# Kernel tuning notes

Measured on AMD Instinct MI355X. Metric: run time of the kernel, lower is better.

The kernel has to match this reference:

```python
import jax, jax.numpy as jnp
import numpy as np

B, C, H, W = 4, 256, 64, 64
CQ = C // 8


def setup_inputs() -> dict:
    key = jax.random.key(0)
    ks = jax.random.split(key, 8)
    s = 0.02
    return {
        "x": jax.random.normal(ks[0], (B, C, H, W), dtype=jnp.float32),
        "Wq": jax.random.normal(ks[1], (CQ, C), dtype=jnp.float32) * s,
        "bq": jax.random.normal(ks[2], (CQ,), dtype=jnp.float32) * s,
        "Wk": jax.random.normal(ks[3], (CQ, C), dtype=jnp.float32) * s,
        "bk": jax.random.normal(ks[4], (CQ,), dtype=jnp.float32) * s,
        "Wv": jax.random.normal(ks[5], (C, C), dtype=jnp.float32) * s,
        "bv": jax.random.normal(ks[6], (C,), dtype=jnp.float32) * s,
        "gamma": jax.random.normal(ks[7], (1,), dtype=jnp.float32) * s,
    }


def reference(x, Wq, bq, Wk, bk, Wv, bv, gamma):
    b, c, h, w = x.shape
    n = h * w
    xf = x.reshape(b, c, n)  # [B,C,N]; 1x1 conv == channel matmul
    q = jnp.einsum("oc,bcn->bno", Wq, xf) + bq  # [B,N,CQ]
    k = jnp.einsum("oc,bcn->bon", Wk, xf) + bk[:, None]  # [B,CQ,N]
    v = jnp.einsum("oc,bcn->bno", Wv, xf) + bv  # [B,N,C]
    attn = jnp.einsum("bnd,bdm->bnm", q, k)  # [B,N,N], unscaled
    attn = jax.nn.softmax(attn, axis=1)  # non-standard axis (over rows)
    out = jnp.einsum("bnm,bmc->bnc", attn, v)  # [B,N,C]
    out = out.transpose(0, 2, 1).reshape(b, c, h, w)
    return gamma * out + x
```

## Files before the change

kernel.cpp:

```cpp
#include <hip/hip_runtime.h>

#define B_ 4
#define C_ 256
#define N_ 4096
#define LOG2E 1.44269504088896340736f

typedef __attribute__((ext_vector_type(8))) short bf16x8;
typedef __attribute__((ext_vector_type(4))) float f32x4;

static __device__ __forceinline__ unsigned short f2bf(float f) {
    unsigned u = __builtin_bit_cast(unsigned, f);
    u += 0x7fffu + ((u >> 16) & 1u);
    return (unsigned short)(u >> 16);
}

static __device__ __forceinline__ float fexp2(float x) {
#if __has_builtin(__builtin_amdgcn_exp2f)
    return __builtin_amdgcn_exp2f(x);
#else
    return exp2f(x);
#endif
}

#define LDS_BARRIER() asm volatile("s_waitcnt lgkmcnt(0)\n\ts_barrier" ::: "memory")

__global__ void k0_wprep(const float* __restrict__ Wq, const float* __restrict__ Wk,
                         const float* __restrict__ Wv, float* __restrict__ WqkT,
                         unsigned short* __restrict__ wvb) {
    int t = blockIdx.x * 256 + threadIdx.x;
    if (t < 256 * 64) {
        int c = t >> 6, o = t & 63;
        WqkT[t] = (o < 32) ? Wq[o * C_ + c] * LOG2E : Wk[(o - 32) * C_ + c];
    }
    int t2 = t - 256 * 64;
    if (t2 >= 0 && t2 < 256 * 256) wvb[t2] = f2bf(Wv[t2]);
}

__global__ __launch_bounds__(256) void k1_qkx(const float* __restrict__ x,
        const float* __restrict__ WqkT, const float* __restrict__ bq,
        const float* __restrict__ bk, unsigned short* __restrict__ qb,
        unsigned short* __restrict__ ktb, unsigned short* __restrict__ xb) {
    __shared__ float red[4][64][64];
    int b = blockIdx.y;
    int n0 = blockIdx.x * 64;
    int l = threadIdx.x & 63, v = threadIdx.x >> 6;
    const float* xp = x + (size_t)b * C_ * N_ + n0 + l;
    unsigned short* xbp = xb + (size_t)b * C_ * N_ + n0 + l;
    float acc[64];
#pragma unroll
    for (int o = 0; o < 64; ++o) acc[o] = 0.0f;
    for (int c = 64 * v; c < 64 * v + 64; ++c) {
        float xv = xp[(size_t)c * N_];
        xbp[(size_t)c * N_] = f2bf(xv);
        const float4* wr4 = (const float4*)(WqkT + c * 64);
#pragma unroll
        for (int o4 = 0; o4 < 16; ++o4) {
            float4 wv = wr4[o4];
            acc[4 * o4 + 0] += wv.x * xv;
            acc[4 * o4 + 1] += wv.y * xv;
            acc[4 * o4 + 2] += wv.z * xv;
            acc[4 * o4 + 3] += wv.w * xv;
        }
    }
#pragma unroll
    for (int o = 0; o < 64; ++o) red[v][l][o] = acc[o];
    __syncthreads();
    int n = threadIdx.x & 63, og = threadIdx.x >> 6;
    int o0 = og * 16;
    unsigned pk[8];
#pragma unroll
    for (int i = 0; i < 8; ++i) {
        int oa = o0 + 2 * i, ob = oa + 1;
        float va = red[0][n][oa] + red[1][n][oa] + red[2][n][oa] + red[3][n][oa];
        float vb = red[0][n][ob] + red[1][n][ob] + red[2][n][ob] + red[3][n][ob];
        if (og < 2) { va += bq[oa] * LOG2E; vb += bq[ob] * LOG2E; }
        else        { va += bk[oa - 32];    vb += bk[ob - 32]; }
        pk[i] = (unsigned)f2bf(va) | ((unsigned)f2bf(vb) << 16);
    }
    unsigned short* dst = (og < 2)
        ? qb + ((size_t)b * N_ + n0 + n) * 32 + o0
        : ktb + ((size_t)b * N_ + n0 + n) * 32 + (o0 - 32);
    ((uint4*)dst)[0] = make_uint4(pk[0], pk[1], pk[2], pk[3]);
    ((uint4*)dst)[1] = make_uint4(pk[4], pk[5], pk[6], pk[7]);
}

__global__ __launch_bounds__(512) void k2_stats(const unsigned short* __restrict__ qb,
        const unsigned short* __restrict__ ktb, float* __restrict__ Wcol) {
    __shared__ float red[64][33];
    int b = blockIdx.y;
    int m0 = blockIdx.x * 64;
    int lane = threadIdx.x & 63, w = threadIdx.x >> 6;
    int r16 = lane & 15, g = lane >> 4;
    const unsigned short* kb = ktb + ((size_t)b * N_ + m0 + r16) * 32 + 8 * g;
    bf16x8 kf0 = *(const bf16x8*)(kb);
    bf16x8 kf1 = *(const bf16x8*)(kb + 16 * 32);
    bf16x8 kf2 = *(const bf16x8*)(kb + 32 * 32);
    bf16x8 kf3 = *(const bf16x8*)(kb + 48 * 32);
    float z0 = 0, z1 = 0, z2 = 0, z3 = 0;
    const unsigned short* qbase = qb + ((size_t)b * N_ + w * 512 + r16) * 32 + 8 * g;
#pragma unroll 2
    for (int n0 = 0; n0 < 512; n0 += 16) {
        bf16x8 qf = *(const bf16x8*)(qbase + (size_t)n0 * 32);
        f32x4 d0 = __builtin_amdgcn_mfma_f32_16x16x32_bf16(qf, kf0, (f32x4){0, 0, 0, 0}, 0, 0, 0);
        f32x4 d1 = __builtin_amdgcn_mfma_f32_16x16x32_bf16(qf, kf1, (f32x4){0, 0, 0, 0}, 0, 0, 0);
        f32x4 d2 = __builtin_amdgcn_mfma_f32_16x16x32_bf16(qf, kf2, (f32x4){0, 0, 0, 0}, 0, 0, 0);
        f32x4 d3 = __builtin_amdgcn_mfma_f32_16x16x32_bf16(qf, kf3, (f32x4){0, 0, 0, 0}, 0, 0, 0);
        z0 += fexp2(d0[0]) + fexp2(d0[1]) + fexp2(d0[2]) + fexp2(d0[3]);
        z1 += fexp2(d1[0]) + fexp2(d1[1]) + fexp2(d1[2]) + fexp2(d1[3]);
        z2 += fexp2(d2[0]) + fexp2(d2[1]) + fexp2(d2[2]) + fexp2(d2[3]);
        z3 += fexp2(d3[0]) + fexp2(d3[1]) + fexp2(d3[2]) + fexp2(d3[3]);
    }
    red[r16][4 * w + g] = z0;
    red[16 + r16][4 * w + g] = z1;
    red[32 + r16][4 * w + g] = z2;
    red[48 + r16][4 * w + g] = z3;
    __syncthreads();
    if (threadIdx.x < 64) {
        float s = 0;
#pragma unroll
        for (int i = 0; i < 32; ++i) s += red[threadIdx.x][i];
        Wcol[(size_t)b * N_ + m0 + threadIdx.x] = 1.0f / s;
    }
}

__global__ __launch_bounds__(512) void k4_y(const unsigned short* __restrict__ qb,
        const unsigned short* __restrict__ ktb, const unsigned short* __restrict__ xb,
        const float* __restrict__ Wcol, unsigned short* __restrict__ Yt,
        float* __restrict__ rowP) {
    __shared__ unsigned short Pl[2][64 * 64];
    __shared__ float rpl[4][64];
    int b = blockIdx.y;
    int n0 = blockIdx.x * 64;
    int lane = threadIdx.x & 63, w = threadIdx.x >> 6;
    int ms = w >> 1, wn = w & 1;
    int r16 = lane & 15, g = lane >> 4;
    int swz = (r16 & 7) << 4;

    const unsigned short* qbp = qb + ((size_t)b * N_ + n0 + 32 * wn + r16) * 32 + 8 * g;
    bf16x8 qf0 = *(const bf16x8*)(qbp);
    bf16x8 qf1 = *(const bf16x8*)(qbp + 16 * 32);
    const unsigned short* kbp = ktb + ((size_t)b * N_ + 16 * ms + r16) * 32 + 8 * g;
    const unsigned short* xbp = xb + ((size_t)b * C_ + 32 * w + r16) * N_ + 8 * g;
    const float* izp = Wcol + (size_t)b * N_ + 16 * ms + 4 * g;

    char* pwbase = (char*)&Pl[0][0] + (32 * wn + r16) * 128 + ((32 * ms + 8 * g) ^ swz);

    f32x4 acc[4][2];
#pragma unroll
    for (int i = 0; i < 4; ++i)
#pragma unroll
        for (int j = 0; j < 2; ++j) acc[i][j] = (f32x4){0, 0, 0, 0};
    float rp0 = 0.0f, rp1 = 0.0f;

    bf16x8 ka = *(const bf16x8*)(kbp);
    bf16x8 xf[2][2], xfn[2][2];
#pragma unroll
    for (int cs = 0; cs < 2; ++cs)
#pragma unroll
        for (int ks = 0; ks < 2; ++ks)
            xf[cs][ks] = *(const bf16x8*)(xbp + (size_t)cs * 16 * N_ + 32 * ks);
    float4 iz = *(const float4*)(izp);
    {
        f32x4 s0 = __builtin_amdgcn_mfma_f32_16x16x32_bf16(ka, qf0, (f32x4){0, 0, 0, 0}, 0, 0, 0);
        f32x4 s1 = __builtin_amdgcn_mfma_f32_16x16x32_bf16(ka, qf1, (f32x4){0, 0, 0, 0}, 0, 0, 0);
        float p00 = fexp2(s0[0]) * iz.x, p01 = fexp2(s0[1]) * iz.y;
        float p02 = fexp2(s0[2]) * iz.z, p03 = fexp2(s0[3]) * iz.w;
        float p10 = fexp2(s1[0]) * iz.x, p11 = fexp2(s1[1]) * iz.y;
        float p12 = fexp2(s1[2]) * iz.z, p13 = fexp2(s1[3]) * iz.w;
        rp0 += p00 + p01 + p02 + p03;
        rp1 += p10 + p11 + p12 + p13;
        *(uint2*)(pwbase) = make_uint2(
            (unsigned)f2bf(p00) | ((unsigned)f2bf(p01) << 16),
            (unsigned)f2bf(p02) | ((unsigned)f2bf(p03) << 16));
        *(uint2*)(pwbase + 16 * 128) = make_uint2(
            (unsigned)f2bf(p10) | ((unsigned)f2bf(p11) << 16),
            (unsigned)f2bf(p12) | ((unsigned)f2bf(p13) << 16));
    }
    LDS_BARRIER();

#pragma unroll 2
    for (int t = 0; t < 64; ++t) {
        int cbuf = t & 1;
        bf16x8 kan = ka;
        float4 izn = iz;
        if (t < 63) {
            size_t m1 = (size_t)(t + 1) * 64;
            kan = *(const bf16x8*)(kbp + m1 * 32);
            izn = *(const float4*)(izp + m1);
#pragma unroll
            for (int cs = 0; cs < 2; ++cs)
#pragma unroll
                for (int ks = 0; ks < 2; ++ks)
                    xfn[cs][ks] = *(const bf16x8*)(xbp + (size_t)cs * 16 * N_ + m1 + 32 * ks);
        }
        const char* prd = (const char*)&Pl[cbuf][0] + r16 * 128;
        bf16x8 pa[4][2];
#pragma unroll
        for (int ns = 0; ns < 4; ++ns)
#pragma unroll
            for (int ks = 0; ks < 2; ++ks)
                pa[ns][ks] = *(const bf16x8*)(prd + ns * 16 * 128 + ((64 * ks + 16 * g) ^ swz));
#pragma unroll
        for (int ns = 0; ns < 4; ++ns)
#pragma unroll
            for (int cs = 0; cs < 2; ++cs)
#pragma unroll
                for (int ks = 0; ks < 2; ++ks)
                    acc[ns][cs] = __builtin_amdgcn_mfma_f32_16x16x32_bf16(
                        pa[ns][ks], xf[cs][ks], acc[ns][cs], 0, 0, 0);
        if (t < 63) {
            f32x4 s0 = __builtin_amdgcn_mfma_f32_16x16x32_bf16(kan, qf0, (f32x4){0, 0, 0, 0}, 0, 0, 0);
            f32x4 s1 = __builtin_amdgcn_mfma_f32_16x16x32_bf16(kan, qf1, (f32x4){0, 0, 0, 0}, 0, 0, 0);
            float p00 = fexp2(s0[0]) * izn.x, p01 = fexp2(s0[1]) * izn.y;
            float p02 = fexp2(s0[2]) * izn.z, p03 = fexp2(s0[3]) * izn.w;
            float p10 = fexp2(s1[0]) * izn.x, p11 = fexp2(s1[1]) * izn.y;
            float p12 = fexp2(s1[2]) * izn.z, p13 = fexp2(s1[3]) * izn.w;
            rp0 += p00 + p01 + p02 + p03;
            rp1 += p10 + p11 + p12 + p13;
            char* pw = pwbase + (cbuf ^ 1) * 8192;
            *(uint2*)(pw) = make_uint2(
                (unsigned)f2bf(p00) | ((unsigned)f2bf(p01) << 16),
                (unsigned)f2bf(p02) | ((unsigned)f2bf(p03) << 16));
            *(uint2*)(pw + 16 * 128) = make_uint2(
                (unsigned)f2bf(p10) | ((unsigned)f2bf(p11) << 16),
                (unsigned)f2bf(p12) | ((unsigned)f2bf(p13) << 16));
        }
        LDS_BARRIER();
        ka = kan;
        iz = izn;
#pragma unroll
        for (int cs = 0; cs < 2; ++cs)
#pragma unroll
            for (int ks = 0; ks < 2; ++ks) xf[cs][ks] = xfn[cs][ks];
    }

    rp0 += __shfl_xor(rp0, 16); rp0 += __shfl_xor(rp0, 32);
    rp1 += __shfl_xor(rp1, 16); rp1 += __shfl_xor(rp1, 32);
    if (g == 0) {
        rpl[ms][32 * wn + r16] = rp0;
        rpl[ms][32 * wn + 16 + r16] = rp1;
    }
    __syncthreads();
    if (threadIdx.x < 64)
        rowP[(size_t)b * N_ + n0 + threadIdx.x] =
            rpl[0][threadIdx.x] + rpl[1][threadIdx.x] + rpl[2][threadIdx.x] + rpl[3][threadIdx.x];

#pragma unroll
    for (int ns = 0; ns < 4; ++ns)
#pragma unroll
        for (int cs = 0; cs < 2; ++cs) {
            int cp = 32 * w + 16 * cs + r16;
            f32x4 a = acc[ns][cs];
#pragma unroll
            for (int r = 0; r < 4; ++r) {
                int n = n0 + 16 * ns + 4 * g + r;
                Yt[((size_t)b * N_ + n) * C_ + cp] = f2bf(a[r]);
            }
        }
}

__global__ __launch_bounds__(256) void k5_out(const float* __restrict__ x,
        const unsigned short* __restrict__ wvb, const unsigned short* __restrict__ Yt,
        const float* __restrict__ rowP, const float* __restrict__ bv,
        const float* __restrict__ gamma, float* __restrict__ out) {
    int b = blockIdx.y;
    int n0 = blockIdx.x * 32;
    int lane = threadIdx.x & 63, w = threadIdx.x >> 6;
    int r16 = lane & 15, g = lane >> 4;
    const unsigned short* wvp = wvb + (64 * w + r16) * C_ + 8 * g;
    const unsigned short* ytp = Yt + ((size_t)b * N_ + n0 + r16) * C_ + 8 * g;

    f32x4 acc[4][2];
#pragma unroll
    for (int i = 0; i < 4; ++i)
#pragma unroll
        for (int j = 0; j < 2; ++j) acc[i][j] = (f32x4){0, 0, 0, 0};

#pragma unroll
    for (int kc = 0; kc < 8; ++kc) {
        bf16x8 yf[2];
#pragma unroll
        for (int ns = 0; ns < 2; ++ns)
            yf[ns] = *(const bf16x8*)(ytp + ns * 16 * C_ + kc * 32);
#pragma unroll
        for (int cs = 0; cs < 4; ++cs) {
            bf16x8 wf = *(const bf16x8*)(wvp + cs * 16 * C_ + kc * 32);
#pragma unroll
            for (int ns = 0; ns < 2; ++ns)
                acc[cs][ns] = __builtin_amdgcn_mfma_f32_16x16x32_bf16(
                    wf, yf[ns], acc[cs][ns], 0, 0, 0);
        }
    }
    float gm = gamma[0];
    float rpv[2];
#pragma unroll
    for (int ns = 0; ns < 2; ++ns) rpv[ns] = rowP[(size_t)b * N_ + n0 + 16 * ns + r16];
#pragma unroll
    for (int cs = 0; cs < 4; ++cs) {
        float4 bvv = *(const float4*)(bv + 64 * w + 16 * cs + 4 * g);
        float bva[4] = {bvv.x, bvv.y, bvv.z, bvv.w};
#pragma unroll
        for (int ns = 0; ns < 2; ++ns)
#pragma unroll
            for (int r = 0; r < 4; ++r) {
                int c = 64 * w + 16 * cs + 4 * g + r;
                int n = n0 + 16 * ns + r16;
                size_t idx = ((size_t)b * C_ + c) * N_ + n;
                out[idx] = gm * (acc[cs][ns][r] + rpv[ns] * bva[r]) + x[idx];
            }
    }
}

extern "C" void kernel_launch(void* const* d_in, const int* in_sizes, int n_in,
                              void* d_out, int out_size, void* d_ws, size_t ws_size,
                              hipStream_t stream) {
    const float* x = (const float*)d_in[0];
    const float* Wq = (const float*)d_in[1];
    const float* bq = (const float*)d_in[2];
    const float* Wk = (const float*)d_in[3];
    const float* bk = (const float*)d_in[4];
    const float* Wv = (const float*)d_in[5];
    const float* bv = (const float*)d_in[6];
    const float* gamma = (const float*)d_in[7];
    float* out = (float*)d_out;

    char* ws = (char*)d_ws;
    unsigned short* qb  = (unsigned short*)(ws);
    unsigned short* ktb = (unsigned short*)(ws + (1u << 20));
    unsigned short* xb  = (unsigned short*)(ws + (2u << 20));
    unsigned short* Yt  = (unsigned short*)(ws + (10u << 20));
    float* Wcol = (float*)(ws + (18u << 20));
    float* WqkT = (float*)(ws + (18u << 20) + (1u << 16));
    unsigned short* wvb = (unsigned short*)(ws + (18u << 20) + (2u << 16));
    float* rowP = (float*)(ws + (18u << 20) + (4u << 16));

    k0_wprep<<<320, 256, 0, stream>>>(Wq, Wk, Wv, WqkT, wvb);
    k1_qkx<<<dim3(N_ / 64, B_), 256, 0, stream>>>(x, WqkT, bq, bk, qb, ktb, xb);
    k2_stats<<<dim3(N_ / 64, B_), 512, 0, stream>>>(qb, ktb, Wcol);
    k4_y<<<dim3(N_ / 64, B_), 512, 0, stream>>>(qb, ktb, xb, Wcol, Yt, rowP);
    k5_out<<<dim3(N_ / 32, B_), 256, 0, stream>>>(x, wvb, Yt, rowP, bv, gamma, out);
}
```

Before: 238.5 us.

## Triple-buffer P tiles in k4_y and deepen global prefetch pipeline

The P tile buffer in k4_y grows from two to three LDS slots. S/exp for a tile is now computed two iterations ahead, and K, Wcol and x fragments are prefetched three to five tiles ahead in rotating registers through a manually unrolled-by-3 loop. The aim is to hide global-load latency and let the exp work overlap the PV MFMAs. The cost is more registers and LDS, and the tail prefetches read past the last tile; those values are never used but may touch memory beyond the buffer.

New measurement: 228.4 us. 4.2% less time.

```diff
diff --git a/kernel.cpp b/kernel.cpp
--- a/kernel.cpp
+++ b/kernel.cpp
@@ -127,7 +127,7 @@
         const unsigned short* __restrict__ ktb, const unsigned short* __restrict__ xb,
         const float* __restrict__ Wcol, unsigned short* __restrict__ Yt,
         float* __restrict__ rowP) {
-    __shared__ unsigned short Pl[2][64 * 64];
+    __shared__ unsigned short Pl[3][64 * 64];
     __shared__ float rpl[4][64];
     int b = blockIdx.y;
     int n0 = blockIdx.x * 64;
@@ -152,48 +152,79 @@
         for (int j = 0; j < 2; ++j) acc[i][j] = (f32x4){0, 0, 0, 0};
     float rp0 = 0.0f, rp1 = 0.0f;
 
-    bf16x8 ka = *(const bf16x8*)(kbp);
-    bf16x8 xf[2][2], xfn[2][2];
+#define S_STEP(KAV, IZV, WJ)                                                          \
+    {                                                                                 \
+        f32x4 s0 = __builtin_amdgcn_mfma_f32_16x16x32_bf16(KAV, qf0, (f32x4){0,0,0,0}, 0, 0, 0); \
+        f32x4 s1 = __builtin_amdgcn_mfma_f32_16x16x32_bf16(KAV, qf1, (f32x4){0,0,0,0}, 0, 0, 0); \
+        float p00 = fexp2(s0[0]) * IZV.x, p01 = fexp2(s0[1]) * IZV.y;                 \
+        float p02 = fexp2(s0[2]) * IZV.z, p03 = fexp2(s0[3]) * IZV.w;                 \
+        float p10 = fexp2(s1[0]) * IZV.x, p11 = fexp2(s1[1]) * IZV.y;                 \
+        float p12 = fexp2(s1[2]) * IZV.z, p13 = fexp2(s1[3]) * IZV.w;                 \
+        rp0 += p00 + p01 + p02 + p03;                                                 \
+        rp1 += p10 + p11 + p12 + p13;                                                 \
+        char* pw = pwbase + (WJ) * 8192;                                              \
+        *(uint2*)(pw) = make_uint2(                                                   \
+            (unsigned)f2bf(p00) | ((unsigned)f2bf(p01) << 16),                        \
+            (unsigned)f2bf(p02) | ((unsigned)f2bf(p03) << 16));                       \
+        *(uint2*)(pw + 16 * 128) = make_uint2(                                        \
+            (unsigned)f2bf(p10) | ((unsigned)f2bf(p11) << 16),                        \
+            (unsigned)f2bf(p12) | ((unsigned)f2bf(p13) << 16));                       \
+    }
+
+    bf16x8 kt0 = *(const bf16x8*)(kbp);
+    bf16x8 kt1 = *(const bf16x8*)(kbp + (size_t)64 * 32);
+    float4 it0 = *(const float4*)(izp);
+    float4 it1 = *(const float4*)(izp + 64);
+    bf16x8 kq0 = *(const bf16x8*)(kbp + (size_t)128 * 32);
+    bf16x8 kq1 = *(const bf16x8*)(kbp + (size_t)192 * 32);
+    bf16x8 kq2 = *(const bf16x8*)(kbp + (size_t)256 * 32);
+    float4 izq0 = *(const float4*)(izp + 128);
+    float4 izq1 = *(const float4*)(izp + 192);
+    float4 izq2 = *(const float4*)(izp + 256);
+    bf16x8 xq0[2][2], xq1[2][2], xq2[2][2];
 #pragma unroll
     for (int cs = 0; cs < 2; ++cs)
 #pragma unroll
-        for (int ks = 0; ks < 2; ++ks)
-            xf[cs][ks] = *(const bf16x8*)(xbp + (size_t)cs * 16 * N_ + 32 * ks);
-    float4 iz = *(const float4*)(izp);
+        for (int ks = 0; ks < 2; ++ks) {
+            xq0[cs][ks] = *(const bf16x8*)(xbp + (size_t)cs * 16 * N_ + 32 * ks);
+            xq1[cs][ks] = *(const bf16x8*)(xbp + (size_t)cs * 16 * N_ + 64 + 32 * ks);
+            xq2[cs][ks] = *(const bf16x8*)(xbp + (size_t)cs * 16 * N_ + 128 + 32 * ks);
+        }
+    S_STEP(kt0, it0, 0);
+    S_STEP(kt1, it1, 1);
+    LDS_BARRIER();
+
+#define BODY(T, J, WJ)                                                                \
+    {                                                                                 \
+        const char* prd = (const char*)&Pl[(J)][0] + r16 * 128;                       \
+        bf16x8 pa[4][2];                                                              \
+        _Pragma("unroll") for (int ns = 0; ns < 4; ++ns)                              \
+            _Pragma("unroll") for (int ks = 0; ks < 2; ++ks)                          \
+                pa[ns][ks] = *(const bf16x8*)(prd + ns * 16 * 128 +                   \
+                                              ((64 * ks + 16 * g) ^ swz));            \
+        if ((T) < 62) S_STEP(kq##J, izq##J, WJ);                                      \
+        _Pragma("unroll") for (int ns = 0; ns < 4; ++ns)                              \
+            _Pragma("unroll") for (int cs = 0; cs < 2; ++cs)                          \
+                _Pragma("unroll") for (int ks = 0; ks < 2; ++ks)                      \
+                    acc[ns][cs] = __builtin_amdgcn_mfma_f32_16x16x32_bf16(            \
+                        pa[ns][ks], xq##J[cs][ks], acc[ns][cs], 0, 0, 0);             \
+        kq##J = *(const bf16x8*)(kbp + (size_t)((T) + 5) * 64 * 32);                  \
+        izq##J = *(const float4*)(izp + (size_t)((T) + 5) * 64);                      \
+        _Pragma("unroll") for (int cs = 0; cs < 2; ++cs)                              \
+            _Pragma("unroll") for (int ks = 0; ks < 2; ++ks)                          \
+                xq##J[cs][ks] = *(const bf16x8*)(xbp + (size_t)cs * 16 * N_ +         \
+                                                 (size_t)((T) + 3) * 64 + 32 * ks);   \
+        LDS_BARRIER();                                                                \
+    }
+
+    for (int u = 0; u < 21; ++u) {
+        int t0 = 3 * u;
+        BODY(t0, 0, 2);
+        BODY(t0 + 1, 1, 0);
+        BODY(t0 + 2, 2, 1);
+    }
     {
-        f32x4 s0 = __builtin_amdgcn_mfma_f32_16x16x32_bf16(ka, qf0, (f32x4){0, 0, 0, 0}, 0, 0, 0);
-        f32x4 s1 = __builtin_amdgcn_mfma_f32_16x16x32_bf16(ka, qf1, (f32x4){0, 0, 0, 0}, 0, 0, 0);
-        float p00 = fexp2(s0[0]) * iz.x, p01 = fexp2(s0[1]) * iz.y;
-        float p02 = fexp2(s0[2]) * iz.z, p03 = fexp2(s0[3]) * iz.w;
-        float p10 = fexp2(s1[0]) * iz.x, p11 = fexp2(s1[1]) * iz.y;
-        float p12 = fexp2(s1[2]) * iz.z, p13 = fexp2(s1[3]) * iz.w;
-        rp0 += p00 + p01 + p02 + p03;
-        rp1 += p10 + p11 + p12 + p13;
-        *(uint2*)(pwbase) = make_uint2(
-            (unsigned)f2bf(p00) | ((unsigned)f2bf(p01) << 16),
-            (unsigned)f2bf(p02) | ((unsigned)f2bf(p03) << 16));
-        *(uint2*)(pwbase + 16 * 128) = make_uint2(
-            (unsigned)f2bf(p10) | ((unsigned)f2bf(p11) << 16),
-            (unsigned)f2bf(p12) | ((unsigned)f2bf(p13) << 16));
-    }
-    LDS_BARRIER();
-
-#pragma unroll 2
-    for (int t = 0; t < 64; ++t) {
-        int cbuf = t & 1;
-        bf16x8 kan = ka;
-        float4 izn = iz;
-        if (t < 63) {
-            size_t m1 = (size_t)(t + 1) * 64;
-            kan = *(const bf16x8*)(kbp + m1 * 32);
-            izn = *(const float4*)(izp + m1);
-#pragma unroll
-            for (int cs = 0; cs < 2; ++cs)
-#pragma unroll
-                for (int ks = 0; ks < 2; ++ks)
-                    xfn[cs][ks] = *(const bf16x8*)(xbp + (size_t)cs * 16 * N_ + m1 + 32 * ks);
-        }
-        const char* prd = (const char*)&Pl[cbuf][0] + r16 * 128;
+        const char* prd = (const char*)&Pl[0][0] + r16 * 128;
         bf16x8 pa[4][2];
 #pragma unroll
         for (int ns = 0; ns < 4; ++ns)
@@ -207,32 +238,10 @@
 #pragma unroll
                 for (int ks = 0; ks < 2; ++ks)
                     acc[ns][cs] = __builtin_amdgcn_mfma_f32_16x16x32_bf16(
-                        pa[ns][ks], xf[cs][ks], acc[ns][cs], 0, 0, 0);
-        if (t < 63) {
-            f32x4 s0 = __builtin_amdgcn_mfma_f32_16x16x32_bf16(kan, qf0, (f32x4){0, 0, 0, 0}, 0, 0, 0);
-            f32x4 s1 = __builtin_amdgcn_mfma_f32_16x16x32_bf16(kan, qf1, (f32x4){0, 0, 0, 0}, 0, 0, 0);
-            float p00 = fexp2(s0[0]) * izn.x, p01 = fexp2(s0[1]) * izn.y;
-            float p02 = fexp2(s0[2]) * izn.z, p03 = fexp2(s0[3]) * izn.w;
-            float p10 = fexp2(s1[0]) * izn.x, p11 = fexp2(s1[1]) * izn.y;
-            float p12 = fexp2(s1[2]) * izn.z, p13 = fexp2(s1[3]) * izn.w;
-            rp0 += p00 + p01 + p02 + p03;
-            rp1 += p10 + p11 + p12 + p13;
-            char* pw = pwbase + (cbuf ^ 1) * 8192;
-            *(uint2*)(pw) = make_uint2(
-                (unsigned)f2bf(p00) | ((unsigned)f2bf(p01) << 16),
-                (unsigned)f2bf(p02) | ((unsigned)f2bf(p03) << 16));
-            *(uint2*)(pw + 16 * 128) = make_uint2(
-                (unsigned)f2bf(p10) | ((unsigned)f2bf(p11) << 16),
-                (unsigned)f2bf(p12) | ((unsigned)f2bf(p13) << 16));
-        }
-        LDS_BARRIER();
-        ka = kan;
-        iz = izn;
-#pragma unroll
-        for (int cs = 0; cs < 2; ++cs)
-#pragma unroll
-            for (int ks = 0; ks < 2; ++ks) xf[cs][ks] = xfn[cs][ks];
-    }
+                        pa[ns][ks], xq0[cs][ks], acc[ns][cs], 0, 0, 0);
+    }
+#undef BODY
+#undef S_STEP
 
     rp0 += __shfl_xor(rp0, 16); rp0 += __shfl_xor(rp0, 32);
     rp1 += __shfl_xor(rp1, 16); rp1 += __shfl_xor(rp1, 32);
```
